# Kernel tuning notes

Measured on AMD Instinct MI355X. Metric: run time of the kernel, lower is better.

## Reference

```python
import jax, jax.numpy as jnp
import numpy as np

N = 262144      # number of points
K = 16          # KNN neighbors -> fixed degree CSR
E = N * K
CLASS_DIM = 40


def setup_inputs() -> dict:
    key = jax.random.key(0)
    ks = jax.random.split(key, 12)
    x = jax.random.normal(ks[0], (N, 3), dtype=jnp.float32)
    indptr = (jnp.arange(N + 1, dtype=jnp.int32) * K)
    indices = jax.random.randint(ks[1], (E,), 0, N, dtype=jnp.int32)

    def xavier(k, fan_out, fan_in):
        bound = np.sqrt(6.0 / (fan_in + fan_out)).astype(np.float32)
        return jax.random.uniform(k, (fan_out, fan_in), dtype=jnp.float32,
                                  minval=-bound, maxval=bound)

    return {
        "x": x, "indptr": indptr, "indices": indices,
        "w1": xavier(ks[2], 64, 3),
        "w2": xavier(ks[3], 64, 64),
        "w3": xavier(ks[4], 64, 64),
        "w4": xavier(ks[5], 128, 64),
        "w5": xavier(ks[6], 1024, 192),
        "wf1": xavier(ks[7], 512, 1024),
        "wf2": xavier(ks[8], 256, 512),
        "wf3": xavier(ks[9], CLASS_DIM, 256),
    }


def reference(x, indptr, indices, w1, w2, w3, w4, w5, wf1, wf2, wf3):
    # mlp1, mlp2 (bias-free Linear + ReLU)
    h = jax.nn.relu(x @ w1.T)          # [N, 64]
    h = jax.nn.relu(h @ w2.T)          # [N, 64]

    # GraphMaxPooling: CSR neighbor max (segment-max over gathered rows)
    n = h.shape[0]
    e = indices.shape[0]
    deg = indptr[1:] - indptr[:-1]                                   # [N]
    seg = jnp.repeat(jnp.arange(n, dtype=jnp.int32), deg,
                     total_repeat_length=e)                          # [E]
    x_gm = jax.ops.segment_max(h[indices], seg, num_segments=n,
                               indices_are_sorted=True)              # [N, 64]

    # mlp3, mlp4
    h3 = jax.nn.relu(h @ w3.T)         # [N, 64]
    h4 = jax.nn.relu(h3 @ w4.T)        # [N, 128]

    # concat neighbor-pooled features with point features, mlp5
    hc = jnp.concatenate([x_gm, h4], axis=1)   # [N, 192]
    h5 = jax.nn.relu(hc @ w5.T)                # [N, 1024]

    # global max pool over points -> [1, 1024]
    g = jnp.max(h5, axis=0, keepdims=True)

    # classifier head (dropout in eval mode = identity)
    f = jax.nn.relu(g @ wf1.T)
    f = jax.nn.relu(f @ wf2.T)
    return f @ wf3.T                            # [1, class_dim]
```

## Files before the change

### kernel.cpp

```cpp
#include <hip/hip_runtime.h>
#include <hip/hip_bf16.h>
#include <stdint.h>

typedef unsigned short u16;
typedef __bf16 bf16x8 __attribute__((ext_vector_type(8)));
typedef float  f32x4  __attribute__((ext_vector_type(4)));
typedef u16    u16x8  __attribute__((ext_vector_type(8)));

__device__ __forceinline__ float bf2f(u16 u) {
    return __uint_as_float(((unsigned)u) << 16);
}
__device__ __forceinline__ u16 f2bf(float f) {
    unsigned u = __float_as_uint(f);
    u += 0x7fffu + ((u >> 16) & 1u);
    return (u16)(u >> 16);
}
__device__ __forceinline__ u16x8 maxu16(u16x8 a, u16x8 b) {
    u16x8 r;
    #pragma unroll
    for (int e = 0; e < 8; ++e) r[e] = a[e] > b[e] ? a[e] : b[e];
    return r;
}

#define MFMA16(a, b, c) __builtin_amdgcn_mfma_f32_16x16x32_bf16(a, b, c, 0, 0, 0)

__device__ u16   h2g_buf[262144 * 64];
__device__ u16   gm_buf [262144 * 64];
__device__ u16   w3b[64 * 64];
__device__ u16   w4b[128 * 64];
__device__ u16   w5b[1024 * 192];
__device__ float g_buf[1024];
__device__ float f1_buf[512];
__device__ float f2_buf[256];

__global__ void k0_zero() { g_buf[threadIdx.x] = 0.f; }

__global__ void kcvt(const float* __restrict__ w3f, const float* __restrict__ w4f,
                     const float* __restrict__ w5f)
{
    int i = blockIdx.x * 256 + threadIdx.x;
    if (i < 4096)        w3b[i]         = f2bf(w3f[i]);
    else if (i < 12288)  w4b[i - 4096]  = f2bf(w4f[i - 4096]);
    else                 w5b[i - 12288] = f2bf(w5f[i - 12288]);
}

__global__ __launch_bounds__(256) void k1_mlp(
    const float* __restrict__ xf, const float* __restrict__ w1f,
    const float* __restrict__ w2f)
{
    __shared__ __align__(16) u16 sw1[64 * 4];
    __shared__ __align__(16) u16 sx [64 * 4];
    __shared__ __align__(16) u16 sw2[64 * 72];
    __shared__ __align__(16) u16 shA[64 * 72];
    __shared__ __align__(16) u16 sh2[64 * 72];

    const int tid = threadIdx.x;
    const int p0  = blockIdx.x * 64;

    for (int i = tid; i < 64 * 64; i += 256)
        sw2[(i >> 6) * 72 + (i & 63)] = f2bf(w2f[i]);
    if (tid < 192) {
        sw1[(tid / 3) * 4 + tid % 3] = f2bf(w1f[tid]);
        sx [(tid / 3) * 4 + tid % 3] = f2bf(xf[p0 * 3 + tid]);
    }
    __syncthreads();

    {
        int m = tid & 63, ng = tid >> 6;
        float x0 = bf2f(sx[m * 4]), x1 = bf2f(sx[m * 4 + 1]), x2 = bf2f(sx[m * 4 + 2]);
        #pragma unroll
        for (int j = 0; j < 16; ++j) {
            int n = ng * 16 + j;
            float s = x0 * bf2f(sw1[n * 4]) + x1 * bf2f(sw1[n * 4 + 1]) + x2 * bf2f(sw1[n * 4 + 2]);
            shA[m * 72 + n] = f2bf(fmaxf(s, 0.f));
        }
    }
    __syncthreads();

    const int lane = tid & 63, w = tid >> 6, q = lane >> 4, l15 = lane & 15;
    const int mrow = 16 * w;

    f32x4 acc2[4];
    #pragma unroll
    for (int nt = 0; nt < 4; ++nt) acc2[nt] = (f32x4){0.f, 0.f, 0.f, 0.f};
    #pragma unroll
    for (int s = 0; s < 2; ++s) {
        bf16x8 a = *(const bf16x8*)&shA[(mrow + l15) * 72 + s * 32 + q * 8];
        #pragma unroll
        for (int nt = 0; nt < 4; ++nt) {
            bf16x8 b = *(const bf16x8*)&sw2[(nt * 16 + l15) * 72 + s * 32 + q * 8];
            acc2[nt] = MFMA16(a, b, acc2[nt]);
        }
    }
    #pragma unroll
    for (int nt = 0; nt < 4; ++nt)
        #pragma unroll
        for (int r = 0; r < 4; ++r) {
            int m = mrow + q * 4 + r;
            sh2[m * 72 + nt * 16 + l15] = f2bf(fmaxf(acc2[nt][r], 0.f));
        }
    __syncthreads();

    {
        int row = tid >> 2, c = (tid & 3) * 16;
        *(u16x8*)&h2g_buf[(size_t)p0 * 64 + tid * 16]     = *(const u16x8*)&sh2[row * 72 + c];
        *(u16x8*)&h2g_buf[(size_t)p0 * 64 + tid * 16 + 8] = *(const u16x8*)&sh2[row * 72 + c + 8];
    }
}

__global__ __launch_bounds__(256) void k2_pool(const int* __restrict__ idx)
{
    const size_t gt = (size_t)blockIdx.x * 256 + threadIdx.x;
    const size_t p  = gt >> 3;
    const int    c  = (threadIdx.x & 7) * 8;

    u16x8 v[16];
    #pragma unroll
    for (int k = 0; k < 16; ++k) {
        int j = idx[p * 16 + k];
        v[k] = *(const u16x8*)&h2g_buf[(size_t)j * 64 + c];
    }
    u16x8 m = v[0];
    #pragma unroll
    for (int k = 1; k < 16; ++k) m = maxu16(m, v[k]);
    *(u16x8*)&gm_buf[p * 64 + c] = m;
}

__global__ __launch_bounds__(256) void k3_fused(int* __restrict__ g)
{
    __shared__ __align__(16) u16 lds[128 * 192 + 2 * 128 * 64];
    u16* sA  = lds;
    u16* sB0 = lds + 24576;
    u16* sB1 = lds + 24576 + 8192;

    const int tid  = threadIdx.x;
    const size_t R0 = (size_t)blockIdx.x * 128;
    const int lane = tid & 63, w = tid >> 6, q = lane >> 4, l15 = lane & 15;
    const int m0w  = (w & 1) * 64, n0w = (w >> 1) * 64;

    #pragma unroll
    for (int c = 0; c < 4; ++c) {
        int i = c * 256 + tid, r = i >> 3, js = i & 7;
        *(u16x8*)&sA[r * 192 + ((js ^ r) & 7) * 8] =
            *(const u16x8*)&gm_buf[(R0 + r) * 64 + js * 8];
        *(u16x8*)&sA[r * 192 + (8 | ((js ^ r) & 7)) * 8] =
            *(const u16x8*)&h2g_buf[(R0 + r) * 64 + js * 8];
    }
    __syncthreads();

    {
        f32x4 a3[2][4];
        #pragma unroll
        for (int mt = 0; mt < 2; ++mt)
            #pragma unroll
            for (int nt = 0; nt < 4; ++nt) a3[mt][nt] = (f32x4){0.f, 0.f, 0.f, 0.f};
        #pragma unroll
        for (int ss = 0; ss < 2; ++ss) {
            int js = ss * 4 + q;
            bf16x8 a[2], b[4];
            #pragma unroll
            for (int mt = 0; mt < 2; ++mt) {
                int r = w * 32 + mt * 16 + l15;
                a[mt] = *(const bf16x8*)&sA[r * 192 + (8 | ((js ^ r) & 7)) * 8];
            }
            #pragma unroll
            for (int nt = 0; nt < 4; ++nt)
                b[nt] = *(const bf16x8*)&w3b[(nt * 16 + l15) * 64 + ss * 32 + q * 8];
            #pragma unroll
            for (int mt = 0; mt < 2; ++mt)
                #pragma unroll
                for (int nt = 0; nt < 4; ++nt)
                    a3[mt][nt] = MFMA16(a[mt], b[nt], a3[mt][nt]);
        }
        #pragma unroll
        for (int mt = 0; mt < 2; ++mt)
            #pragma unroll
            for (int nt = 0; nt < 4; ++nt)
                #pragma unroll
                for (int r = 0; r < 4; ++r) {
                    int m = w * 32 + mt * 16 + q * 4 + r;
                    int n = nt * 16 + l15;
                    sA[m * 192 + (16 | (((n >> 3) ^ m) & 7)) * 8 + (n & 7)] =
                        f2bf(fmaxf(a3[mt][nt][r], 0.f));
                }
    }

    {
        f32x4 a4[2][8];
        #pragma unroll
        for (int mt = 0; mt < 2; ++mt)
            #pragma unroll
            for (int nt = 0; nt < 8; ++nt) a4[mt][nt] = (f32x4){0.f, 0.f, 0.f, 0.f};
        #pragma unroll
        for (int ss = 0; ss < 2; ++ss) {
            int js = ss * 4 + q;
            bf16x8 a[2];
            #pragma unroll
            for (int mt = 0; mt < 2; ++mt) {
                int r = w * 32 + mt * 16 + l15;
                a[mt] = *(const bf16x8*)&sA[r * 192 + (16 | ((js ^ r) & 7)) * 8];
            }
            #pragma unroll
            for (int nt = 0; nt < 8; ++nt) {
                bf16x8 b = *(const bf16x8*)&w4b[(nt * 16 + l15) * 64 + ss * 32 + q * 8];
                #pragma unroll
                for (int mt = 0; mt < 2; ++mt)
                    a4[mt][nt] = MFMA16(a[mt], b, a4[mt][nt]);
            }
        }
        #pragma unroll
        for (int mt = 0; mt < 2; ++mt)
            #pragma unroll
            for (int nt = 0; nt < 8; ++nt)
                #pragma unroll
                for (int r = 0; r < 4; ++r) {
                    int m  = w * 32 + mt * 16 + q * 4 + r;
                    int n4 = nt * 16 + l15;
                    int j  = 8 + (n4 >> 3);
                    int p  = (j & 24) | ((j ^ m) & 7);
                    sA[m * 192 + p * 8 + (n4 & 7)] = f2bf(fmaxf(a4[mt][nt][r], 0.f));
                }
    }
    __syncthreads();

    bf16x8 areg[3][2][4];
    #pragma unroll
    for (int kt = 0; kt < 3; ++kt)
        #pragma unroll
        for (int ss = 0; ss < 2; ++ss) {
            int js = ss * 4 + q;
            #pragma unroll
            for (int mt = 0; mt < 4; ++mt) {
                int r = m0w + mt * 16 + l15;
                int p = (kt * 8) | ((js ^ r) & 7);
                areg[kt][ss][mt] = *(const bf16x8*)&sA[r * 192 + p * 8];
            }
        }

    u16x8 v[4];
    #pragma unroll
    for (int c = 0; c < 4; ++c) {
        int i = c * 256 + tid, r = i >> 3, js = i & 7;
        v[c] = *(const u16x8*)&w5b[(size_t)r * 192 + js * 8];
    }
    #pragma unroll
    for (int c = 0; c < 4; ++c) {
        int i = c * 256 + tid, r = i >> 3, js = i & 7;
        *(u16x8*)&sB0[r * 64 + ((js ^ r) & 7) * 8] = v[c];
    }

    int s = 0;
    for (int bn = 0; bn < 8; ++bn) {
        f32x4 acc[4][4];
        #pragma unroll
        for (int mt = 0; mt < 4; ++mt)
            #pragma unroll
            for (int nt = 0; nt < 4; ++nt) acc[mt][nt] = (f32x4){0.f, 0.f, 0.f, 0.f};

        #pragma unroll
        for (int kt = 0; kt < 3; ++kt, ++s) {
            if (s < 23) {
                int s1 = s + 1, bn1 = s1 / 3, kt1 = s1 - bn1 * 3;
                #pragma unroll
                for (int c = 0; c < 4; ++c) {
                    int i = c * 256 + tid, r = i >> 3, js = i & 7;
                    v[c] = *(const u16x8*)&w5b[(size_t)(bn1 * 128 + r) * 192 + kt1 * 64 + js * 8];
                }
            }
            __syncthreads();
            const u16* sBc = (s & 1) ? sB1 : sB0;
            bf16x8 b[2][4];
            #pragma unroll
            for (int ss = 0; ss < 2; ++ss) {
                int js = ss * 4 + q;
                #pragma unroll
                for (int nt = 0; nt < 4; ++nt) {
                    int r = n0w + nt * 16 + l15;
                    b[ss][nt] = *(const bf16x8*)&sBc[r * 64 + ((js ^ r) & 7) * 8];
                }
            }
            #pragma unroll
            for (int ss = 0; ss < 2; ++ss)
                #pragma unroll
                for (int mt = 0; mt < 4; ++mt)
                    #pragma unroll
                    for (int nt = 0; nt < 4; ++nt)
                        acc[mt][nt] = MFMA16(areg[kt][ss][mt], b[ss][nt], acc[mt][nt]);
            if (s < 23) {
                u16* sBn = (s & 1) ? sB0 : sB1;
                #pragma unroll
                for (int c = 0; c < 4; ++c) {
                    int i = c * 256 + tid, r = i >> 3, js = i & 7;
                    *(u16x8*)&sBn[r * 64 + ((js ^ r) & 7) * 8] = v[c];
                }
            }
        }

        #pragma unroll
        for (int nt = 0; nt < 4; ++nt) {
            float mx = 0.f;
            #pragma unroll
            for (int mt = 0; mt < 4; ++mt)
                #pragma unroll
                for (int r = 0; r < 4; ++r) mx = fmaxf(mx, acc[mt][nt][r]);
            mx = fmaxf(mx, __shfl_xor(mx, 16, 64));
            mx = fmaxf(mx, __shfl_xor(mx, 32, 64));
            if (q == 0) {
                int col = bn * 128 + n0w + nt * 16 + l15;
                atomicMax(&g[col], __float_as_int(mx));
            }
        }
    }
}

__global__ void k4_f1(const float* __restrict__ wf1)
{
    int r = blockIdx.x, l = threadIdx.x;
    float s = 0.f;
    #pragma unroll
    for (int i = 0; i < 16; ++i) s += wf1[r * 1024 + i * 64 + l] * g_buf[i * 64 + l];
    #pragma unroll
    for (int o = 32; o; o >>= 1) s += __shfl_down(s, o, 64);
    if (!l) f1_buf[r] = fmaxf(s, 0.f);
}
__global__ void k4_f2(const float* __restrict__ wf2)
{
    int r = blockIdx.x, l = threadIdx.x;
    float s = 0.f;
    #pragma unroll
    for (int i = 0; i < 8; ++i) s += wf2[r * 512 + i * 64 + l] * f1_buf[i * 64 + l];
    #pragma unroll
    for (int o = 32; o; o >>= 1) s += __shfl_down(s, o, 64);
    if (!l) f2_buf[r] = fmaxf(s, 0.f);
}
__global__ void k4_out(const float* __restrict__ wf3, float* __restrict__ out)
{
    int r = blockIdx.x, l = threadIdx.x;
    float s = 0.f;
    #pragma unroll
    for (int i = 0; i < 4; ++i) s += wf3[r * 256 + i * 64 + l] * f2_buf[i * 64 + l];
    #pragma unroll
    for (int o = 32; o; o >>= 1) s += __shfl_down(s, o, 64);
    if (!l) out[r] = s;
}

extern "C" void kernel_launch(void* const* d_in, const int* in_sizes, int n_in,
                              void* d_out, int out_size, void* d_ws, size_t ws_size,
                              hipStream_t stream)
{
    (void)in_sizes; (void)n_in; (void)out_size; (void)d_ws; (void)ws_size;
    const float* x   = (const float*)d_in[0];
    const int*   idx = (const int*)d_in[2];
    const float* w1  = (const float*)d_in[3];
    const float* w2  = (const float*)d_in[4];
    const float* w3  = (const float*)d_in[5];
    const float* w4  = (const float*)d_in[6];
    const float* w5  = (const float*)d_in[7];
    const float* wf1 = (const float*)d_in[8];
    const float* wf2 = (const float*)d_in[9];
    const float* wf3 = (const float*)d_in[10];

    float* gptr;
    hipGetSymbolAddress((void**)&gptr, HIP_SYMBOL(g_buf));

    k0_zero <<<1, 1024, 0, stream>>>();
    kcvt    <<<816, 256, 0, stream>>>(w3, w4, w5);
    k1_mlp  <<<262144 / 64, 256, 0, stream>>>(x, w1, w2);
    k2_pool <<<262144 * 8 / 256, 256, 0, stream>>>(idx);
    k3_fused<<<262144 / 128, 256, 0, stream>>>((int*)gptr);
    k4_f1   <<<512, 64, 0, stream>>>(wf1);
    k4_f2   <<<256, 64, 0, stream>>>(wf2);
    k4_out  <<<40, 64, 0, stream>>>(wf3, (float*)d_out);
}
```

Before: 460.5 us.

## Make mlp5 kernel persistent with register-resident w5 slices and double-buffered row tiles

Restructures the fused mlp3/mlp4/mlp5 kernel into a persistent grid of 256 blocks of 512 threads. Each block holds a 256-column slice of w5 in registers and iterates over 32 row tiles, prefetching the next tile into a second LDS buffer. Running column maxima stay in registers, so each block issues one set of atomicMax at the end instead of one per tile. It removes the per-tile re-streaming of w5 through LDS and the extra syncs and atomics. In exchange, mlp3/mlp4 are recomputed and the activations reloaded once per column group (4x), and register pressure limits occupancy.

Result: slower. 481.0 us (+4.5%).

```diff
diff --git a/kernel.cpp b/kernel.cpp
--- a/kernel.cpp
+++ b/kernel.cpp
@@ -19,6 +19,12 @@
     u16x8 r;
     #pragma unroll
     for (int e = 0; e < 8; ++e) r[e] = a[e] > b[e] ? a[e] : b[e];
+    return r;
+}
+__device__ __forceinline__ f32x4 maxf4(f32x4 a, f32x4 b) {
+    f32x4 r;
+    #pragma unroll
+    for (int e = 0; e < 4; ++e) r[e] = fmaxf(a[e], b[e]);
     return r;
 }
 
@@ -126,190 +132,174 @@
     *(u16x8*)&gm_buf[p * 64 + c] = m;
 }
 
-__global__ __launch_bounds__(256) void k3_fused(int* __restrict__ g)
-{
-    __shared__ __align__(16) u16 lds[128 * 192 + 2 * 128 * 64];
-    u16* sA  = lds;
-    u16* sB0 = lds + 24576;
-    u16* sB1 = lds + 24576 + 8192;
+__global__ __launch_bounds__(512, 2) void k3_fused(int* __restrict__ gout)
+{
+    __shared__ __align__(16) u16 lds[61440];
+    u16* sA0 = lds;
+    u16* sA1 = lds + 24576;
+    u16* sw3 = lds + 49152;
+    u16* sw4 = lds + 53248;
 
     const int tid  = threadIdx.x;
-    const size_t R0 = (size_t)blockIdx.x * 128;
     const int lane = tid & 63, w = tid >> 6, q = lane >> 4, l15 = lane & 15;
-    const int m0w  = (w & 1) * 64, n0w = (w >> 1) * 64;
-
-    #pragma unroll
-    for (int c = 0; c < 4; ++c) {
-        int i = c * 256 + tid, r = i >> 3, js = i & 7;
-        *(u16x8*)&sA[r * 192 + ((js ^ r) & 7) * 8] =
-            *(const u16x8*)&gm_buf[(R0 + r) * 64 + js * 8];
-        *(u16x8*)&sA[r * 192 + (8 | ((js ^ r) & 7)) * 8] =
-            *(const u16x8*)&h2g_buf[(R0 + r) * 64 + js * 8];
+    const int mw   = w & 1, nw = w >> 1;
+    const int cg   = blockIdx.x >> 6;
+    const int brow = blockIdx.x & 63;
+    const int bcol0 = cg * 256 + nw * 64;
+
+    {
+        int r = tid >> 3, js = tid & 7;
+        *(u16x8*)&sw3[r * 64 + ((js ^ r) & 7) * 8] = *(const u16x8*)&w3b[r * 64 + js * 8];
+        #pragma unroll
+        for (int c = 0; c < 2; ++c) {
+            int i = c * 512 + tid, r4 = i >> 3, j4 = i & 7;
+            *(u16x8*)&sw4[r4 * 64 + ((j4 ^ r4) & 7) * 8] = *(const u16x8*)&w4b[r4 * 64 + j4 * 8];
+        }
+    }
+
+    bf16x8 b5[6][4];
+    #pragma unroll
+    for (int s = 0; s < 6; ++s)
+        #pragma unroll
+        for (int nt = 0; nt < 4; ++nt)
+            b5[s][nt] = *(const bf16x8*)&w5b[(size_t)(bcol0 + nt * 16 + l15) * 192 + s * 32 + q * 8];
+
+    {
+        size_t R0 = (size_t)brow * 32 * 128;
+        #pragma unroll
+        for (int c = 0; c < 2; ++c) {
+            int i = c * 512 + tid, r = i >> 3, js = i & 7;
+            *(u16x8*)&sA0[r * 192 + ((js ^ r) & 7) * 8] =
+                *(const u16x8*)&gm_buf[(R0 + r) * 64 + js * 8];
+            *(u16x8*)&sA0[r * 192 + (8 | ((js ^ r) & 7)) * 8] =
+                *(const u16x8*)&h2g_buf[(R0 + r) * 64 + js * 8];
+        }
     }
     __syncthreads();
 
-    {
-        f32x4 a3[2][4];
-        #pragma unroll
-        for (int mt = 0; mt < 2; ++mt)
-            #pragma unroll
-            for (int nt = 0; nt < 4; ++nt) a3[mt][nt] = (f32x4){0.f, 0.f, 0.f, 0.f};
-        #pragma unroll
-        for (int ss = 0; ss < 2; ++ss) {
-            int js = ss * 4 + q;
-            bf16x8 a[2], b[4];
-            #pragma unroll
-            for (int mt = 0; mt < 2; ++mt) {
-                int r = w * 32 + mt * 16 + l15;
-                a[mt] = *(const bf16x8*)&sA[r * 192 + (8 | ((js ^ r) & 7)) * 8];
+    f32x4 rmax[4];
+    #pragma unroll
+    for (int nt = 0; nt < 4; ++nt) rmax[nt] = (f32x4){0.f, 0.f, 0.f, 0.f};
+
+    u16* pc = sA0;
+    u16* pn = sA1;
+
+    #pragma unroll 1
+    for (int t = 0; t < 32; ++t) {
+        u16x8 vg[2], vh[2];
+        if (t < 31) {
+            size_t R1 = (size_t)(brow * 32 + t + 1) * 128;
+            #pragma unroll
+            for (int c = 0; c < 2; ++c) {
+                int i = c * 512 + tid, r = i >> 3, js = i & 7;
+                vg[c] = *(const u16x8*)&gm_buf[(R1 + r) * 64 + js * 8];
+                vh[c] = *(const u16x8*)&h2g_buf[(R1 + r) * 64 + js * 8];
+            }
+        }
+
+        {
+            f32x4 a3[4];
+            #pragma unroll
+            for (int nt = 0; nt < 4; ++nt) a3[nt] = (f32x4){0.f, 0.f, 0.f, 0.f};
+            #pragma unroll
+            for (int ss = 0; ss < 2; ++ss) {
+                int js = ss * 4 + q, r = w * 16 + l15;
+                bf16x8 a = *(const bf16x8*)&pc[r * 192 + (8 | ((js ^ r) & 7)) * 8];
+                #pragma unroll
+                for (int nt = 0; nt < 4; ++nt) {
+                    int rw = nt * 16 + l15;
+                    bf16x8 b = *(const bf16x8*)&sw3[rw * 64 + ((js ^ rw) & 7) * 8];
+                    a3[nt] = MFMA16(a, b, a3[nt]);
+                }
             }
             #pragma unroll
             for (int nt = 0; nt < 4; ++nt)
-                b[nt] = *(const bf16x8*)&w3b[(nt * 16 + l15) * 64 + ss * 32 + q * 8];
-            #pragma unroll
-            for (int mt = 0; mt < 2; ++mt)
-                #pragma unroll
-                for (int nt = 0; nt < 4; ++nt)
-                    a3[mt][nt] = MFMA16(a[mt], b[nt], a3[mt][nt]);
-        }
-        #pragma unroll
-        for (int mt = 0; mt < 2; ++mt)
-            #pragma unroll
-            for (int nt = 0; nt < 4; ++nt)
                 #pragma unroll
                 for (int r = 0; r < 4; ++r) {
-                    int m = w * 32 + mt * 16 + q * 4 + r;
+                    int m = w * 16 + q * 4 + r;
                     int n = nt * 16 + l15;
-                    sA[m * 192 + (16 | (((n >> 3) ^ m) & 7)) * 8 + (n & 7)] =
-                        f2bf(fmaxf(a3[mt][nt][r], 0.f));
-                }
-    }
-
-    {
-        f32x4 a4[2][8];
-        #pragma unroll
-        for (int mt = 0; mt < 2; ++mt)
-            #pragma unroll
-            for (int nt = 0; nt < 8; ++nt) a4[mt][nt] = (f32x4){0.f, 0.f, 0.f, 0.f};
-        #pragma unroll
-        for (int ss = 0; ss < 2; ++ss) {
-            int js = ss * 4 + q;
-            bf16x8 a[2];
-            #pragma unroll
-            for (int mt = 0; mt < 2; ++mt) {
-                int r = w * 32 + mt * 16 + l15;
-                a[mt] = *(const bf16x8*)&sA[r * 192 + (16 | ((js ^ r) & 7)) * 8];
-            }
-            #pragma unroll
-            for (int nt = 0; nt < 8; ++nt) {
-                bf16x8 b = *(const bf16x8*)&w4b[(nt * 16 + l15) * 64 + ss * 32 + q * 8];
-                #pragma unroll
-                for (int mt = 0; mt < 2; ++mt)
-                    a4[mt][nt] = MFMA16(a[mt], b, a4[mt][nt]);
-            }
-        }
-        #pragma unroll
-        for (int mt = 0; mt < 2; ++mt)
+                    pc[m * 192 + (16 | (((n >> 3) ^ m) & 7)) * 8 + (n & 7)] =
+                        f2bf(fmaxf(a3[nt][r], 0.f));
+                }
+        }
+
+        {
+            f32x4 a4[8];
+            #pragma unroll
+            for (int nt = 0; nt < 8; ++nt) a4[nt] = (f32x4){0.f, 0.f, 0.f, 0.f};
+            #pragma unroll
+            for (int ss = 0; ss < 2; ++ss) {
+                int js = ss * 4 + q, r = w * 16 + l15;
+                bf16x8 a = *(const bf16x8*)&pc[r * 192 + (16 | ((js ^ r) & 7)) * 8];
+                #pragma unroll
+                for (int nt = 0; nt < 8; ++nt) {
+                    int rw = nt * 16 + l15;
+                    bf16x8 b = *(const bf16x8*)&sw4[rw * 64 + ((js ^ rw) & 7) * 8];
+                    a4[nt] = MFMA16(a, b, a4[nt]);
+                }
+            }
             #pragma unroll
             for (int nt = 0; nt < 8; ++nt)
                 #pragma unroll
                 for (int r = 0; r < 4; ++r) {
-                    int m  = w * 32 + mt * 16 + q * 4 + r;
+                    int m  = w * 16 + q * 4 + r;
                     int n4 = nt * 16 + l15;
                     int j  = 8 + (n4 >> 3);
                     int p  = (j & 24) | ((j ^ m) & 7);
-                    sA[m * 192 + p * 8 + (n4 & 7)] = f2bf(fmaxf(a4[mt][nt][r], 0.f));
-                }
-    }
-    __syncthreads();
-
-    bf16x8 areg[3][2][4];
-    #pragma unroll
-    for (int kt = 0; kt < 3; ++kt)
-        #pragma unroll
-        for (int ss = 0; ss < 2; ++ss) {
-            int js = ss * 4 + q;
-            #pragma unroll
-            for (int mt = 0; mt < 4; ++mt) {
-                int r = m0w + mt * 16 + l15;
-                int p = (kt * 8) | ((js ^ r) & 7);
-                areg[kt][ss][mt] = *(const bf16x8*)&sA[r * 192 + p * 8];
-            }
-        }
-
-    u16x8 v[4];
-    #pragma unroll
-    for (int c = 0; c < 4; ++c) {
-        int i = c * 256 + tid, r = i >> 3, js = i & 7;
-        v[c] = *(const u16x8*)&w5b[(size_t)r * 192 + js * 8];
-    }
-    #pragma unroll
-    for (int c = 0; c < 4; ++c) {
-        int i = c * 256 + tid, r = i >> 3, js = i & 7;
-        *(u16x8*)&sB0[r * 64 + ((js ^ r) & 7) * 8] = v[c];
-    }
-
-    int s = 0;
-    for (int bn = 0; bn < 8; ++bn) {
-        f32x4 acc[4][4];
-        #pragma unroll
-        for (int mt = 0; mt < 4; ++mt)
-            #pragma unroll
-            for (int nt = 0; nt < 4; ++nt) acc[mt][nt] = (f32x4){0.f, 0.f, 0.f, 0.f};
-
-        #pragma unroll
-        for (int kt = 0; kt < 3; ++kt, ++s) {
-            if (s < 23) {
-                int s1 = s + 1, bn1 = s1 / 3, kt1 = s1 - bn1 * 3;
-                #pragma unroll
-                for (int c = 0; c < 4; ++c) {
-                    int i = c * 256 + tid, r = i >> 3, js = i & 7;
-                    v[c] = *(const u16x8*)&w5b[(size_t)(bn1 * 128 + r) * 192 + kt1 * 64 + js * 8];
-                }
-            }
-            __syncthreads();
-            const u16* sBc = (s & 1) ? sB1 : sB0;
-            bf16x8 b[2][4];
-            #pragma unroll
-            for (int ss = 0; ss < 2; ++ss) {
-                int js = ss * 4 + q;
-                #pragma unroll
-                for (int nt = 0; nt < 4; ++nt) {
-                    int r = n0w + nt * 16 + l15;
-                    b[ss][nt] = *(const bf16x8*)&sBc[r * 64 + ((js ^ r) & 7) * 8];
-                }
-            }
-            #pragma unroll
-            for (int ss = 0; ss < 2; ++ss)
+                    pc[m * 192 + p * 8 + (n4 & 7)] = f2bf(fmaxf(a4[nt][r], 0.f));
+                }
+        }
+        __syncthreads();
+
+        {
+            f32x4 acc[4][4];
+            #pragma unroll
+            for (int mt = 0; mt < 4; ++mt)
+                #pragma unroll
+                for (int nt = 0; nt < 4; ++nt) acc[mt][nt] = (f32x4){0.f, 0.f, 0.f, 0.f};
+            #pragma unroll
+            for (int s = 0; s < 6; ++s) {
+                int j = s * 4 + q;
+                bf16x8 a[4];
+                #pragma unroll
+                for (int mt = 0; mt < 4; ++mt) {
+                    int r = mw * 64 + mt * 16 + l15;
+                    int p = (j & 24) | ((j ^ r) & 7);
+                    a[mt] = *(const bf16x8*)&pc[r * 192 + p * 8];
+                }
                 #pragma unroll
                 for (int mt = 0; mt < 4; ++mt)
                     #pragma unroll
                     for (int nt = 0; nt < 4; ++nt)
-                        acc[mt][nt] = MFMA16(areg[kt][ss][mt], b[ss][nt], acc[mt][nt]);
-            if (s < 23) {
-                u16* sBn = (s & 1) ? sB0 : sB1;
-                #pragma unroll
-                for (int c = 0; c < 4; ++c) {
-                    int i = c * 256 + tid, r = i >> 3, js = i & 7;
-                    *(u16x8*)&sBn[r * 64 + ((js ^ r) & 7) * 8] = v[c];
-                }
-            }
-        }
-
-        #pragma unroll
-        for (int nt = 0; nt < 4; ++nt) {
-            float mx = 0.f;
-            #pragma unroll
-            for (int mt = 0; mt < 4; ++mt)
-                #pragma unroll
-                for (int r = 0; r < 4; ++r) mx = fmaxf(mx, acc[mt][nt][r]);
-            mx = fmaxf(mx, __shfl_xor(mx, 16, 64));
-            mx = fmaxf(mx, __shfl_xor(mx, 32, 64));
-            if (q == 0) {
-                int col = bn * 128 + n0w + nt * 16 + l15;
-                atomicMax(&g[col], __float_as_int(mx));
-            }
-        }
+                        acc[mt][nt] = MFMA16(a[mt], b5[s][nt], acc[mt][nt]);
+            }
+            #pragma unroll
+            for (int nt = 0; nt < 4; ++nt)
+                #pragma unroll
+                for (int mt = 0; mt < 4; ++mt)
+                    rmax[nt] = maxf4(rmax[nt], acc[mt][nt]);
+        }
+
+        if (t < 31) {
+            #pragma unroll
+            for (int c = 0; c < 2; ++c) {
+                int i = c * 512 + tid, r = i >> 3, js = i & 7;
+                *(u16x8*)&pn[r * 192 + ((js ^ r) & 7) * 8]       = vg[c];
+                *(u16x8*)&pn[r * 192 + (8 | ((js ^ r) & 7)) * 8] = vh[c];
+            }
+        }
+        __syncthreads();
+        u16* tmp = pc; pc = pn; pn = tmp;
+    }
+
+    #pragma unroll
+    for (int nt = 0; nt < 4; ++nt) {
+        float mx = fmaxf(fmaxf(rmax[nt][0], rmax[nt][1]),
+                         fmaxf(rmax[nt][2], rmax[nt][3]));
+        mx = fmaxf(mx, __shfl_xor(mx, 16, 64));
+        mx = fmaxf(mx, __shfl_xor(mx, 32, 64));
+        if (q == 0)
+            atomicMax(&gout[bcol0 + nt * 16 + l15], __float_as_int(mx));
     }
 }
 
@@ -367,7 +357,7 @@
     kcvt    <<<816, 256, 0, stream>>>(w3, w4, w5);
     k1_mlp  <<<262144 / 64, 256, 0, stream>>>(x, w1, w2);
     k2_pool <<<262144 * 8 / 256, 256, 0, stream>>>(idx);
-    k3_fused<<<262144 / 128, 256, 0, stream>>>((int*)gptr);
+    k3_fused<<<256, 512, 0, stream>>>((int*)gptr);
     k4_f1   <<<512, 64, 0, stream>>>(wf1);
     k4_f2   <<<256, 64, 0, stream>>>(wf2);
     k4_out  <<<40, 64, 0, stream>>>(wf3, (float*)d_out);
```
